# Kernel optimization log

Hardware: AMD Instinct MI355X
Metric: run time of the kernel (lower is better)

The kernel has to match this reference:

```python
import jax, jax.numpy as jnp
import numpy as np

B, S, D, H, CLIP = 4, 1024, 1024, 16, 64
DH = D // H

def setup_inputs() -> dict:
    key = jax.random.key(0)
    ks = jax.random.split(key, 10)
    sc = 1.0 / np.sqrt(D)
    return {
        "queries": jax.random.normal(ks[0], (B, S, D), jnp.float32),
        "keys": jax.random.normal(ks[1], (B, S, D), jnp.float32),
        "values": jax.random.normal(ks[2], (B, S, D), jnp.float32),
        "valid_lens": jax.random.randint(ks[3], (B,), 0, S),
        "Wq": jax.random.normal(ks[4], (D, D), jnp.float32) * sc,
        "Wk": jax.random.normal(ks[5], (D, D), jnp.float32) * sc,
        "Wv": jax.random.normal(ks[6], (D, D), jnp.float32) * sc,
        "Wo": jax.random.normal(ks[7], (D, D), jnp.float32) * sc,
        "rpr_k": jax.random.normal(ks[8], (2 * CLIP + 1, DH), jnp.float32),
        "rpr_v": jax.random.normal(ks[9], (2 * CLIP + 1, DH), jnp.float32),
    }

def reference(queries, keys, values, valid_lens, Wq, Wk, Wv, Wo, rpr_k, rpr_v):
    # project and split heads: [B,S,D] -> [B,H,S,DH]
    def split(x, W):
        return (x @ W).reshape(B, S, H, DH).transpose(0, 2, 1, 3)
    q = split(queries, Wq)
    k = split(keys, Wk)
    v = split(values, Wv)
    # relative position indices [S,S] in [0, 2*CLIP]
    dist = jnp.arange(S)[None, :] - jnp.arange(S)[:, None]
    dist = jnp.clip(dist, -CLIP, CLIP) + CLIP
    pos_k = rpr_k[dist]  # [S,S,DH]
    pos_v = rpr_v[dist]  # [S,S,DH]
    # content scores + relative-position key bias
    scores = jnp.einsum('bhqd,bhkd->bhqk', q, k)
    scores = scores + jnp.einsum('bhqd,qkd->bhqk', q, pos_k)
    scores = scores / jnp.sqrt(jnp.asarray(DH, q.dtype))
    # masked softmax: positions >= valid_len set to -1e6 (matches torch code)
    key_mask = jnp.arange(S)[None, None, None, :] < valid_lens[:, None, None, None]
    scores = jnp.where(key_mask, scores, jnp.asarray(-1e6, scores.dtype))
    attn = jax.nn.softmax(scores, axis=-1)  # [B,H,S,S]
    # value aggregation + relative-position value bias
    out = jnp.einsum('bhqk,bhkd->bhqd', attn, v)
    out = out + jnp.einsum('bhqk,qkd->bhqd', attn, pos_v)
    out = out.transpose(0, 2, 1, 3).reshape(B, S, D)
    return out @ Wo
```

## Files before the change

kernel.cpp:

```cpp
#include <hip/hip_runtime.h>
#include <stdint.h>
#include <math.h>

#define BB 4
#define SS 1024
#define DD 1024
#define HH 16
#define DHH 64
#define NCLIP 64
#define NCC 129
#define NCP 160
#define QRSTR 148
#define M0F 20.0f

typedef __bf16 bf16;
typedef __bf16 bf16x8 __attribute__((ext_vector_type(8)));
typedef float f32x4 __attribute__((ext_vector_type(4)));

__device__ __forceinline__ void gload_lds16(const void* g, void* l) {
  __builtin_amdgcn_global_load_lds((const __attribute__((address_space(1))) void*)g,
                                   (__attribute__((address_space(3))) void*)l, 16, 0, 0);
}

struct TpArgs { const float* w[4]; bf16* wt[4]; };
__global__ __launch_bounds__(256) void transpose_pack_w(TpArgs args) {
  const float* __restrict__ W = args.w[blockIdx.z];
  bf16* __restrict__ Wt = args.wt[blockIdx.z];
  __shared__ float tile[32][33];
  int tx = threadIdx.x, ty = threadIdx.y;
  int n0 = blockIdx.x * 32, k0 = blockIdx.y * 32;
#pragma unroll
  for (int i = 0; i < 4; i++)
    tile[ty + i * 8][tx] = W[(size_t)(k0 + ty + i * 8) * DD + n0 + tx];
  __syncthreads();
#pragma unroll
  for (int i = 0; i < 4; i++)
    Wt[(size_t)(n0 + ty + i * 8) * DD + k0 + tx] = (bf16)tile[tx][ty + i * 8];
}

struct CvtArgs { const float* in[3]; bf16* out[3]; int skip[3]; };
__global__ __launch_bounds__(256) void f32_to_bf16_3(CvtArgs args, const int* __restrict__ vlens) {
  const int z = blockIdx.z;
  if (args.skip[z]) {
    int row0 = (blockIdx.x * 2) & 1023;
    int b = (blockIdx.x * 2) >> 10;
    int vl = vlens[b];
    if (vl > 0 && row0 >= vl) return;
  }
  const float* __restrict__ in = args.in[z];
  bf16* __restrict__ out = args.out[z];
  size_t i = ((size_t)blockIdx.x * 256 + threadIdx.x) * 8;
  f32x4 v0 = *(const f32x4*)(in + i);
  f32x4 v1 = *(const f32x4*)(in + i + 4);
  bf16x8 o;
#pragma unroll
  for (int j = 0; j < 4; j++) { o[j] = (bf16)v0[j]; o[j + 4] = (bf16)v1[j]; }
  *(bf16x8*)(out + i) = o;
}

struct GemmArgs { const bf16* a[3]; const bf16* bt[3]; void* c[3]; float sc[3]; int skip[3]; };
template <bool SPLIT>
__global__ __launch_bounds__(256) void gemm128(GemmArgs args, const int* __restrict__ vlens) {
  const int z = blockIdx.z;
  const int m0 = blockIdx.y * 128, n0 = blockIdx.x * 128;
  if (args.skip[z]) {
    int vl = vlens[m0 >> 10];
    if (vl > 0 && (m0 & 1023) >= vl) return;
  }
  const bf16* __restrict__ A  = args.a[z];
  const bf16* __restrict__ Bt = args.bt[z];
  void* __restrict__ Cv = args.c[z];
  const float scale = args.sc[z];
  __shared__ __align__(16) bf16 As[128][32];
  __shared__ __align__(16) bf16 Bs[128][32];
  const int tid = threadIdx.x, lane = tid & 63, wv = tid >> 6;
  const int wr = wv >> 1, wc = wv & 1;
  const int l15 = lane & 15, l4 = lane >> 4;
  const int srow = lane >> 2, scol = (lane & 3) * 8;
  f32x4 z4 = {0.f, 0.f, 0.f, 0.f};
  f32x4 acc[4][4];
#pragma unroll
  for (int i = 0; i < 4; i++)
#pragma unroll
    for (int j = 0; j < 4; j++) acc[i][j] = z4;

  for (int k0 = 0; k0 < DD; k0 += 32) {
    gload_lds16(A  + (size_t)(m0 + wv * 16 + srow) * DD + k0 + scol,      &As[wv * 16][0]);
    gload_lds16(A  + (size_t)(m0 + 64 + wv * 16 + srow) * DD + k0 + scol, &As[64 + wv * 16][0]);
    gload_lds16(Bt + (size_t)(n0 + wv * 16 + srow) * DD + k0 + scol,      &Bs[wv * 16][0]);
    gload_lds16(Bt + (size_t)(n0 + 64 + wv * 16 + srow) * DD + k0 + scol, &Bs[64 + wv * 16][0]);
    __syncthreads();
    bf16x8 af[4], bfv[4];
#pragma unroll
    for (int i = 0; i < 4; i++) {
      af[i]  = *(const bf16x8*)&As[wr * 64 + i * 16 + l15][l4 * 8];
      bfv[i] = *(const bf16x8*)&Bs[wc * 64 + i * 16 + l15][l4 * 8];
    }
#pragma unroll
    for (int mi = 0; mi < 4; mi++)
#pragma unroll
      for (int ni = 0; ni < 4; ni++)
        acc[mi][ni] = __builtin_amdgcn_mfma_f32_16x16x32_bf16(af[mi], bfv[ni], acc[mi][ni], 0, 0, 0);
    __syncthreads();
  }
#pragma unroll
  for (int mi = 0; mi < 4; mi++)
#pragma unroll
    for (int ni = 0; ni < 4; ni++)
#pragma unroll
      for (int r = 0; r < 4; r++) {
        int m = m0 + wr * 64 + mi * 16 + l4 * 4 + r;
        int n = n0 + wc * 64 + ni * 16 + l15;
        float val = acc[mi][ni][r] * scale;
        if (SPLIT) {
          ((bf16*)Cv)[((((size_t)(m >> 10) * HH + (n >> 6)) * SS) + (m & 1023)) * DHH + (n & 63)] =
              (bf16)val;
        } else {
          ((float*)Cv)[(size_t)m * DD + n] = val;
        }
      }
}

__global__ __launch_bounds__(256) void gemm_bf16_final(const bf16* __restrict__ A,
                                                       const bf16* __restrict__ Bt,
                                                       float* __restrict__ C) {
  __shared__ __align__(16) bf16 As[64][32];
  __shared__ __align__(16) bf16 Bs[128][32];
  const int tid = threadIdx.x, lane = tid & 63, wv = tid >> 6;
  const int l15 = lane & 15, l4 = lane >> 4;
  const int m0 = blockIdx.y * 64, n0 = blockIdx.x * 128;
  const int srow = lane >> 2, scol = (lane & 3) * 8;
  f32x4 z4 = {0.f, 0.f, 0.f, 0.f};
  f32x4 acc[4][2];
#pragma unroll
  for (int i = 0; i < 4; i++) { acc[i][0] = z4; acc[i][1] = z4; }

  for (int k0 = 0; k0 < DD; k0 += 32) {
    gload_lds16(A + (size_t)(m0 + wv * 16 + srow) * DD + k0 + scol, &As[wv * 16][0]);
    gload_lds16(Bt + (size_t)(n0 + wv * 32 + srow) * DD + k0 + scol, &Bs[wv * 32][0]);
    gload_lds16(Bt + (size_t)(n0 + wv * 32 + 16 + srow) * DD + k0 + scol, &Bs[wv * 32 + 16][0]);
    __syncthreads();
    bf16x8 af[4], bfv[2];
#pragma unroll
    for (int i = 0; i < 4; i++) af[i] = *(const bf16x8*)&As[i * 16 + l15][l4 * 8];
#pragma unroll
    for (int i = 0; i < 2; i++) bfv[i] = *(const bf16x8*)&Bs[wv * 32 + i * 16 + l15][l4 * 8];
#pragma unroll
    for (int mi = 0; mi < 4; mi++)
#pragma unroll
      for (int ni = 0; ni < 2; ni++)
        acc[mi][ni] = __builtin_amdgcn_mfma_f32_16x16x32_bf16(af[mi], bfv[ni], acc[mi][ni], 0, 0, 0);
    __syncthreads();
  }
#pragma unroll
  for (int mi = 0; mi < 4; mi++)
#pragma unroll
    for (int ni = 0; ni < 2; ni++)
#pragma unroll
      for (int r = 0; r < 4; r++) {
        int m = m0 + mi * 16 + l4 * 4 + r;
        int n = n0 + wv * 32 + ni * 16 + l15;
        C[(size_t)m * DD + n] = acc[mi][ni][r];
      }
}

__global__ __launch_bounds__(256) void vh_transpose(const bf16* __restrict__ Vh,
                                                    bf16* __restrict__ VhT,
                                                    const int* __restrict__ vlens) {
  __shared__ bf16 til[64][65];
  int bh = blockIdx.y;
  int s0 = blockIdx.x * 64;
  int vl = vlens[bh >> 4];
  if (vl > 0 && s0 >= vl + 32) return;
  const bf16* src = Vh + (size_t)bh * SS * DHH + (size_t)s0 * DHH;
  for (int i = threadIdx.x; i < 64 * 64; i += 256) {
    int r = i >> 6, cc = i & 63;
    til[r][cc] = src[(size_t)r * DHH + cc];
  }
  __syncthreads();
  bf16* dst = VhT + (size_t)bh * DHH * SS + s0;
  for (int i = threadIdx.x; i < 64 * 64; i += 256) {
    int d = i >> 6, cc = i & 63;
    dst[(size_t)d * SS + cc] = til[cc][d];
  }
}

__global__ void prep_tables(const float* __restrict__ rpr_v, const float* __restrict__ rpr_k,
                            bf16* __restrict__ rvT, bf16* __restrict__ rkP) {
  int i = blockIdx.x * 256 + threadIdx.x;
  if (i < DHH * NCP) {
    int d = i / NCP, c = i - d * NCP;
    rvT[i] = (c < NCC) ? (bf16)rpr_v[(size_t)c * DHH + d] : (bf16)0.f;
  }
  if (i < 144 * 64) {
    rkP[i] = (i < NCC * DHH) ? (bf16)rpr_k[i] : (bf16)0.f;
  }
}

__global__ __launch_bounds__(256, 4) void attn_mfma(
    const bf16* __restrict__ Qh, const bf16* __restrict__ Kh, const bf16* __restrict__ VhT,
    const bf16* __restrict__ rkP, const int* __restrict__ valid_lens,
    const bf16* __restrict__ rvT, bf16* __restrict__ Obh) {
  __shared__ __align__(16) char arena[4][10240];
  const int tid = threadIdx.x, lane = tid & 63, w = tid >> 6;
  const int l15 = lane & 15, l4 = lane >> 4;
  const int b = blockIdx.z, h = blockIdx.y, bh = b * HH + h;
  const int q0 = blockIdx.x * 64 + w * 16;
  const int vlen = valid_lens[b];
  const float mval = (vlen == 0) ? 0.f : -30000.f;
  char* base = arena[w];
  bf16* QRs = (bf16*)base;
  _Float16* SBand = (_Float16*)(base + 4736);
  bf16* Pl = (bf16*)(base + 8832);

  const bf16* Qbase = Qh + ((size_t)bh * SS + q0) * DHH;
  bf16x8 qa0 = *(const bf16x8*)(Qbase + (size_t)l15 * DHH + l4 * 8);
  bf16x8 qa1 = *(const bf16x8*)(Qbase + (size_t)l15 * DHH + 32 + l4 * 8);
  const bf16* Kbase = Kh + (size_t)bh * SS * DHH;
  const bf16* Vbase = VhT + (size_t)bh * DHH * SS;
  f32x4 z = {0.f, 0.f, 0.f, 0.f};

#pragma unroll
  for (int ni = 0; ni < 9; ni++) {
    const bf16* rp = rkP + (size_t)(ni * 16 + l15) * DHH + l4 * 8;
    bf16x8 b0 = *(const bf16x8*)(rp);
    bf16x8 b1 = *(const bf16x8*)(rp + 32);
    f32x4 acc = __builtin_amdgcn_mfma_f32_16x16x32_bf16(qa0, b0, z, 0, 0, 0);
    acc = __builtin_amdgcn_mfma_f32_16x16x32_bf16(qa1, b1, acc, 0, 0, 0);
#pragma unroll
    for (int r = 0; r < 4; r++)
      QRs[(l4 * 4 + r) * QRSTR + ni * 16 + l15] = (bf16)acc[r];
  }
  {
    _Float16 ninf = (_Float16)(-65504.f);
    for (int i = lane; i < 16 * 128; i += 64) SBand[i] = ninf;
  }

  float biasLo[4], biasHi[4];
#pragma unroll
  for (int r = 0; r < 4; r++) {
    biasLo[r] = (float)QRs[(l4 * 4 + r) * QRSTR + 0];
    biasHi[r] = (float)QRs[(l4 * 4 + r) * QRSTR + 128];
  }

  float l_lane[4], slo[4], shi[4];
#pragma unroll
  for (int r = 0; r < 4; r++) { l_lane[r] = 0.f; slo[r] = 0.f; shi[r] = 0.f; }
  f32x4 acco[4];
#pragma unroll
  for (int i = 0; i < 4; i++) acco[i] = z;

  const int kf = (vlen > 0) ? (vlen & ~31) : 0;
  const int kte = (vlen > 0) ? ((vlen + 31) & ~31) : SS;
  int bs = q0 - 94; bs = (bs < 0) ? 0 : ((bs + 31) & ~31);
  int be = (q0 + 110) & ~31; if (be > SS) be = SS;
  const int p1 = (bs < kf) ? bs : kf;
  const int p2 = (be < kf) ? be : kf;

#define QK_LOADS                                                              \
    const bf16* kp = Kbase + (size_t)(ks + l15) * DHH + l4 * 8;               \
    bf16x8 kf00 = *(const bf16x8*)(kp);                                       \
    bf16x8 kf01 = *(const bf16x8*)(kp + 32);                                  \
    bf16x8 kf10 = *(const bf16x8*)(kp + 16 * DHH);                            \
    bf16x8 kf11 = *(const bf16x8*)(kp + 16 * DHH + 32);                       \
    f32x4 a0 = __builtin_amdgcn_mfma_f32_16x16x32_bf16(qa0, kf00, z, 0, 0, 0);\
    a0 = __builtin_amdgcn_mfma_f32_16x16x32_bf16(qa1, kf01, a0, 0, 0, 0);     \
    f32x4 a1 = __builtin_amdgcn_mfma_f32_16x16x32_bf16(qa0, kf10, z, 0, 0, 0);\
    a1 = __builtin_amdgcn_mfma_f32_16x16x32_bf16(qa1, kf11, a1, 0, 0, 0);

#define PV_STEP                                                               \
    bf16x8 pa = *(const bf16x8*)&Pl[l15 * 40 + l4 * 8];                       \
    const bf16* vp = Vbase + (size_t)l15 * SS + ks + l4 * 8;                  \
    acco[0] = __builtin_amdgcn_mfma_f32_16x16x32_bf16(pa, *(const bf16x8*)(vp), acco[0], 0, 0, 0);                    \
    acco[1] = __builtin_amdgcn_mfma_f32_16x16x32_bf16(pa, *(const bf16x8*)(vp + (size_t)16 * SS), acco[1], 0, 0, 0);  \
    acco[2] = __builtin_amdgcn_mfma_f32_16x16x32_bf16(pa, *(const bf16x8*)(vp + (size_t)32 * SS), acco[2], 0, 0, 0);  \
    acco[3] = __builtin_amdgcn_mfma_f32_16x16x32_bf16(pa, *(const bf16x8*)(vp + (size_t)48 * SS), acco[3], 0, 0, 0);

  for (int ks = 0; ks < p1; ks += 32) {
    QK_LOADS
#pragma unroll
    for (int sub = 0; sub < 2; sub++) {
      const f32x4 a = sub ? a1 : a0;
#pragma unroll
      for (int r = 0; r < 4; r++) {
        float p = __expf(a[r] + biasLo[r] - M0F);
        l_lane[r] += p; slo[r] += p;
        Pl[(l4 * 4 + r) * 40 + sub * 16 + l15] = (bf16)p;
      }
    }
    PV_STEP
  }
  for (int ks = p1; ks < p2; ks += 32) {
    QK_LOADS
#pragma unroll
    for (int sub = 0; sub < 2; sub++) {
      const f32x4 a = sub ? a1 : a0;
      const int kg = ks + sub * 16 + l15;
#pragma unroll
      for (int r = 0; r < 4; r++) {
        const int qloc = l4 * 4 + r;
        int dlt = kg - q0 - qloc;
        int c = (dlt < -NCLIP ? -NCLIP : (dlt > NCLIP ? NCLIP : dlt)) + NCLIP;
        float s = a[r] + (float)QRs[qloc * QRSTR + c];
        if (dlt > -64 && dlt < 64) SBand[qloc * 128 + dlt + 63] = (_Float16)s;
        float p = __expf(s - M0F);
        l_lane[r] += p;
        slo[r] += (dlt <= -64) ? p : 0.f;
        shi[r] += (dlt >= 64) ? p : 0.f;
        Pl[qloc * 40 + sub * 16 + l15] = (bf16)p;
      }
    }
    PV_STEP
  }
  for (int ks = p2; ks < kf; ks += 32) {
    QK_LOADS
#pragma unroll
    for (int sub = 0; sub < 2; sub++) {
      const f32x4 a = sub ? a1 : a0;
#pragma unroll
      for (int r = 0; r < 4; r++) {
        float p = __expf(a[r] + biasHi[r] - M0F);
        l_lane[r] += p; shi[r] += p;
        Pl[(l4 * 4 + r) * 40 + sub * 16 + l15] = (bf16)p;
      }
    }
    PV_STEP
  }
  for (int ks = kf; ks < kte; ks += 32) {
    const int rel = ks - q0;
    const int mode = (rel <= -95) ? 0 : (rel >= 79) ? 1 : 2;
    QK_LOADS
#pragma unroll
    for (int sub = 0; sub < 2; sub++) {
      const f32x4 a = sub ? a1 : a0;
      const int kg = ks + sub * 16 + l15;
      const bool msk = (kg >= vlen);
      if (mode == 0) {
#pragma unroll
        for (int r = 0; r < 4; r++) {
          float s = msk ? mval : (a[r] + biasLo[r]);
          float p = __expf(s - M0F);
          l_lane[r] += p; slo[r] += p;
          Pl[(l4 * 4 + r) * 40 + sub * 16 + l15] = (bf16)p;
        }
      } else if (mode == 1) {
#pragma unroll
        for (int r = 0; r < 4; r++) {
          float s = msk ? mval : (a[r] + biasHi[r]);
          float p = __expf(s - M0F);
          l_lane[r] += p; shi[r] += p;
          Pl[(l4 * 4 + r) * 40 + sub * 16 + l15] = (bf16)p;
        }
      } else {
#pragma unroll
        for (int r = 0; r < 4; r++) {
          const int qloc = l4 * 4 + r;
          int dlt = kg - q0 - qloc;
          int c = (dlt < -NCLIP ? -NCLIP : (dlt > NCLIP ? NCLIP : dlt)) + NCLIP;
          float s = a[r] + (float)QRs[qloc * QRSTR + c];
          if (msk) s = mval;
          if (dlt > -64 && dlt < 64) SBand[qloc * 128 + dlt + 63] = (_Float16)s;
          float p = __expf(s - M0F);
          l_lane[r] += p;
          slo[r] += (dlt <= -64) ? p : 0.f;
          shi[r] += (dlt >= 64) ? p : 0.f;
          Pl[qloc * 40 + sub * 16 + l15] = (bf16)p;
        }
      }
    }
    PV_STEP
  }
#undef QK_LOADS
#undef PV_STEP

  float* li_s   = (float*)(base + 8832);
  float* a0_s   = (float*)(base + 8896);
  float* a128_s = (float*)(base + 8960);
  float li_r[4];
#pragma unroll
  for (int r = 0; r < 4; r++) {
    const int qloc = l4 * 4 + r;
    float lt = l_lane[r], so = slo[r], sh = shi[r];
    lt += __shfl_xor(lt, 1, 64); so += __shfl_xor(so, 1, 64); sh += __shfl_xor(sh, 1, 64);
    lt += __shfl_xor(lt, 2, 64); so += __shfl_xor(so, 2, 64); sh += __shfl_xor(sh, 2, 64);
    lt += __shfl_xor(lt, 4, 64); so += __shfl_xor(so, 4, 64); sh += __shfl_xor(sh, 4, 64);
    lt += __shfl_xor(lt, 8, 64); so += __shfl_xor(so, 8, 64); sh += __shfl_xor(sh, 8, 64);
    float li = 1.f / lt;
    li_r[r] = li;
    if (l15 == 0) { li_s[qloc] = li; a0_s[qloc] = so * li; a128_s[qloc] = sh * li; }
  }
  bf16* AWs = (bf16*)base;
  for (int row = 0; row < 16; row++) {
    float li = li_s[row], a0 = a0_s[row], a128 = a128_s[row];
#pragma unroll
    for (int j = 0; j < 3; j++) {
      int c = lane + 64 * j;
      if (c < 160) {
        float val;
        if (c == 0) val = a0;
        else if (c == 128) val = a128;
        else if (c < 128) val = __expf((float)SBand[row * 128 + c - 1] - M0F) * li;
        else val = 0.f;
        AWs[row * 168 + c] = (bf16)val;
      }
    }
  }
  f32x4 acc2[4];
#pragma unroll
  for (int i = 0; i < 4; i++) acc2[i] = z;
#pragma unroll
  for (int kk = 0; kk < 5; kk++) {
    bf16x8 af = *(const bf16x8*)&AWs[l15 * 168 + kk * 32 + l4 * 8];
#pragma unroll
    for (int ni = 0; ni < 4; ni++) {
      bf16x8 bv = *(const bf16x8*)(rvT + (size_t)(ni * 16 + l15) * NCP + kk * 32 + l4 * 8);
      acc2[ni] = __builtin_amdgcn_mfma_f32_16x16x32_bf16(af, bv, acc2[ni], 0, 0, 0);
    }
  }
#pragma unroll
  for (int ni = 0; ni < 4; ni++)
#pragma unroll
    for (int r = 0; r < 4; r++) {
      int qg = q0 + l4 * 4 + r;
      Obh[((size_t)b * SS + qg) * DD + h * DHH + ni * 16 + l15] =
          (bf16)(acco[ni][r] * li_r[r] + acc2[ni][r]);
    }
}

extern "C" void kernel_launch(void* const* d_in, const int* in_sizes, int n_in,
                              void* d_out, int out_size, void* d_ws, size_t ws_size,
                              hipStream_t stream) {
  (void)in_sizes; (void)n_in; (void)out_size; (void)ws_size;
  const float* queries = (const float*)d_in[0];
  const float* keys    = (const float*)d_in[1];
  const float* values  = (const float*)d_in[2];
  const int*   vlens   = (const int*)d_in[3];
  const float* Wq = (const float*)d_in[4];
  const float* Wk = (const float*)d_in[5];
  const float* Wv = (const float*)d_in[6];
  const float* Wo = (const float*)d_in[7];
  const float* rpr_k = (const float*)d_in[8];
  const float* rpr_v = (const float*)d_in[9];

  char* ws = (char*)d_ws;
  const size_t MB = 1024 * 1024;
  bf16* Wtq  = (bf16*)(ws + 0 * MB);
  bf16* Wtk  = (bf16*)(ws + 2 * MB);
  bf16* Wtv  = (bf16*)(ws + 4 * MB);
  bf16* Wto  = (bf16*)(ws + 6 * MB);
  bf16* Qh   = (bf16*)(ws + 8 * MB);
  bf16* Kh   = (bf16*)(ws + 16 * MB);
  bf16* Vh   = (bf16*)(ws + 24 * MB);
  bf16* VhT  = (bf16*)(ws + 32 * MB);
  bf16* Qb   = (bf16*)(ws + 40 * MB);
  bf16* Kb   = (bf16*)(ws + 48 * MB);
  bf16* Vb   = (bf16*)(ws + 56 * MB);
  bf16* Obh  = (bf16*)(ws + 64 * MB);
  bf16* rvT  = (bf16*)(ws + 72 * MB);
  bf16* rkP  = (bf16*)(ws + 73 * MB);

  TpArgs tp; tp.w[0] = Wq; tp.w[1] = Wk; tp.w[2] = Wv; tp.w[3] = Wo;
  tp.wt[0] = Wtq; tp.wt[1] = Wtk; tp.wt[2] = Wtv; tp.wt[3] = Wto;
  transpose_pack_w<<<dim3(32, 32, 4), dim3(32, 8), 0, stream>>>(tp);

  CvtArgs cv; cv.in[0] = queries; cv.in[1] = keys; cv.in[2] = values;
  cv.out[0] = Qb; cv.out[1] = Kb; cv.out[2] = Vb;
  cv.skip[0] = 0; cv.skip[1] = 1; cv.skip[2] = 1;
  f32_to_bf16_3<<<dim3(2048, 1, 3), 256, 0, stream>>>(cv, vlens);

  GemmArgs gp;
  gp.a[0] = Qb; gp.a[1] = Kb; gp.a[2] = Vb;
  gp.bt[0] = Wtq; gp.bt[1] = Wtk; gp.bt[2] = Wtv;
  gp.c[0] = (void*)Qh; gp.c[1] = (void*)Kh; gp.c[2] = (void*)Vh;
  gp.sc[0] = 0.125f; gp.sc[1] = 1.0f; gp.sc[2] = 1.0f;
  gp.skip[0] = 0; gp.skip[1] = 1; gp.skip[2] = 1;
  gemm128<true><<<dim3(8, 32, 3), 256, 0, stream>>>(gp, vlens);

  vh_transpose<<<dim3(16, 64), 256, 0, stream>>>(Vh, VhT, vlens);
  prep_tables<<<dim3(40), 256, 0, stream>>>(rpr_v, rpr_k, rvT, rkP);
  attn_mfma<<<dim3(16, HH, BB), 256, 0, stream>>>(Qh, Kh, VhT, rkP, vlens, rvT, Obh);
  gemm_bf16_final<<<dim3(8, 64), 256, 0, stream>>>(Obh, Wto, (float*)d_out);
}
```

Before: 127.7 us.

## Split attention key range across wave pairs and merge partials via LDS atomics

```diff
diff --git a/kernel.cpp b/kernel.cpp
--- a/kernel.cpp
+++ b/kernel.cpp
@@ -201,17 +201,22 @@
     const bf16* __restrict__ Qh, const bf16* __restrict__ Kh, const bf16* __restrict__ VhT,
     const bf16* __restrict__ rkP, const int* __restrict__ valid_lens,
     const bf16* __restrict__ rvT, bf16* __restrict__ Obh) {
-  __shared__ __align__(16) char arena[4][10240];
+  __shared__ __align__(16) char arena[2][15744];
   const int tid = threadIdx.x, lane = tid & 63, w = tid >> 6;
+  const int pair = w >> 1, khalf = w & 1;
   const int l15 = lane & 15, l4 = lane >> 4;
   const int b = blockIdx.z, h = blockIdx.y, bh = b * HH + h;
-  const int q0 = blockIdx.x * 64 + w * 16;
+  const int q0 = blockIdx.x * 32 + pair * 16;
   const int vlen = valid_lens[b];
   const float mval = (vlen == 0) ? 0.f : -30000.f;
-  char* base = arena[w];
+  char* base = arena[pair];
   bf16* QRs = (bf16*)base;
-  _Float16* SBand = (_Float16*)(base + 4736);
-  bf16* Pl = (bf16*)(base + 8832);
+  bf16* Pl = (bf16*)(base + 4736 + khalf * 1280);
+  _Float16* SBand = (_Float16*)(base + 7296);
+  float* Oacc = (float*)(base + 11392);
+  float* lsum_l  = (float*)(base + 15488);
+  float* lsum_lo = (float*)(base + 15552);
+  float* lsum_hi = (float*)(base + 15616);
 
   const bf16* Qbase = Qh + ((size_t)bh * SS + q0) * DHH;
   bf16x8 qa0 = *(const bf16x8*)(Qbase + (size_t)l15 * DHH + l4 * 8);
@@ -220,8 +225,7 @@
   const bf16* Vbase = VhT + (size_t)bh * DHH * SS;
   f32x4 z = {0.f, 0.f, 0.f, 0.f};
 
-#pragma unroll
-  for (int ni = 0; ni < 9; ni++) {
+  for (int ni = khalf ? 5 : 0; ni < (khalf ? 9 : 5); ni++) {
     const bf16* rp = rkP + (size_t)(ni * 16 + l15) * DHH + l4 * 8;
     bf16x8 b0 = *(const bf16x8*)(rp);
     bf16x8 b1 = *(const bf16x8*)(rp + 32);
@@ -233,8 +237,11 @@
   }
   {
     _Float16 ninf = (_Float16)(-65504.f);
-    for (int i = lane; i < 16 * 128; i += 64) SBand[i] = ninf;
-  }
+    for (int i = lane + khalf * 1024; i < khalf * 1024 + 1024; i += 64) SBand[i] = ninf;
+    for (int i = lane + khalf * 64; i < 1024; i += 128) Oacc[i] = 0.f;
+    if (khalf == 0 && lane < 48) lsum_l[lane] = 0.f;
+  }
+  __syncthreads();
 
   float biasLo[4], biasHi[4];
 #pragma unroll
@@ -250,12 +257,17 @@
 #pragma unroll
   for (int i = 0; i < 4; i++) acco[i] = z;
 
-  const int kf = (vlen > 0) ? (vlen & ~31) : 0;
   const int kte = (vlen > 0) ? ((vlen + 31) & ~31) : SS;
+  const int kf  = (vlen > 0) ? (vlen & ~31) : 0;
   int bs = q0 - 94; bs = (bs < 0) ? 0 : ((bs + 31) & ~31);
   int be = (q0 + 110) & ~31; if (be > SS) be = SS;
-  const int p1 = (bs < kf) ? bs : kf;
-  const int p2 = (be < kf) ? be : kf;
+  const int P1 = (bs < kf) ? bs : kf;
+  const int P2 = (be < kf) ? be : kf;
+  const int kmid = ((kte + 63) >> 6) << 5;
+  const int kb = khalf ? kmid : 0;
+  const int ke = khalf ? kte : kmid;
+#define IMAX(a, bq) ((a) > (bq) ? (a) : (bq))
+#define IMIN(a, bq) ((a) < (bq) ? (a) : (bq))
 
 #define QK_LOADS                                                              \
     const bf16* kp = Kbase + (size_t)(ks + l15) * DHH + l4 * 8;               \
@@ -276,7 +288,7 @@
     acco[2] = __builtin_amdgcn_mfma_f32_16x16x32_bf16(pa, *(const bf16x8*)(vp + (size_t)32 * SS), acco[2], 0, 0, 0);  \
     acco[3] = __builtin_amdgcn_mfma_f32_16x16x32_bf16(pa, *(const bf16x8*)(vp + (size_t)48 * SS), acco[3], 0, 0, 0);
 
-  for (int ks = 0; ks < p1; ks += 32) {
+  for (int ks = kb, e = IMIN(P1, ke); ks < e; ks += 32) {
     QK_LOADS
 #pragma unroll
     for (int sub = 0; sub < 2; sub++) {
@@ -290,7 +302,7 @@
     }
     PV_STEP
   }
-  for (int ks = p1; ks < p2; ks += 32) {
+  for (int ks = IMAX(kb, P1), e = IMIN(P2, ke); ks < e; ks += 32) {
     QK_LOADS
 #pragma unroll
     for (int sub = 0; sub < 2; sub++) {
@@ -312,7 +324,7 @@
     }
     PV_STEP
   }
-  for (int ks = p2; ks < kf; ks += 32) {
+  for (int ks = IMAX(kb, P2), e = IMIN(kf, ke); ks < e; ks += 32) {
     QK_LOADS
 #pragma unroll
     for (int sub = 0; sub < 2; sub++) {
@@ -326,7 +338,7 @@
     }
     PV_STEP
   }
-  for (int ks = kf; ks < kte; ks += 32) {
+  for (int ks = IMAX(kb, kf), e = IMIN(kte, ke); ks < e; ks += 32) {
     const int rel = ks - q0;
     const int mode = (rel <= -95) ? 0 : (rel >= 79) ? 1 : 2;
     QK_LOADS
@@ -373,10 +385,6 @@
 #undef QK_LOADS
 #undef PV_STEP
 
-  float* li_s   = (float*)(base + 8832);
-  float* a0_s   = (float*)(base + 8896);
-  float* a128_s = (float*)(base + 8960);
-  float li_r[4];
 #pragma unroll
   for (int r = 0; r < 4; r++) {
     const int qloc = l4 * 4 + r;
@@ -385,46 +393,62 @@
     lt += __shfl_xor(lt, 2, 64); so += __shfl_xor(so, 2, 64); sh += __shfl_xor(sh, 2, 64);
     lt += __shfl_xor(lt, 4, 64); so += __shfl_xor(so, 4, 64); sh += __shfl_xor(sh, 4, 64);
     lt += __shfl_xor(lt, 8, 64); so += __shfl_xor(so, 8, 64); sh += __shfl_xor(sh, 8, 64);
-    float li = 1.f / lt;
-    li_r[r] = li;
-    if (l15 == 0) { li_s[qloc] = li; a0_s[qloc] = so * li; a128_s[qloc] = sh * li; }
-  }
+    if (l15 == 0) {
+      atomicAdd(&lsum_l[qloc], lt);
+      atomicAdd(&lsum_lo[qloc], so);
+      atomicAdd(&lsum_hi[qloc], sh);
+    }
+#pragma unroll
+    for (int ni = 0; ni < 4; ni++)
+      atomicAdd(&Oacc[qloc * 64 + ni * 16 + l15], acco[ni][r]);
+  }
+  __syncthreads();
+
   bf16* AWs = (bf16*)base;
-  for (int row = 0; row < 16; row++) {
-    float li = li_s[row], a0 = a0_s[row], a128 = a128_s[row];
+  for (int row = khalf * 8; row < khalf * 8 + 8; row++) {
+    float li = 1.f / lsum_l[row];
+    float a0v = lsum_lo[row] * li, a128v = lsum_hi[row] * li;
 #pragma unroll
     for (int j = 0; j < 3; j++) {
       int c = lane + 64 * j;
       if (c < 160) {
         float val;
-        if (c == 0) val = a0;
-        else if (c == 128) val = a128;
+        if (c == 0) val = a0v;
+        else if (c == 128) val = a128v;
         else if (c < 128) val = __expf((float)SBand[row * 128 + c - 1] - M0F) * li;
         else val = 0.f;
         AWs[row * 168 + c] = (bf16)val;
       }
     }
   }
-  f32x4 acc2[4];
-#pragma unroll
-  for (int i = 0; i < 4; i++) acc2[i] = z;
-#pragma unroll
-  for (int kk = 0; kk < 5; kk++) {
-    bf16x8 af = *(const bf16x8*)&AWs[l15 * 168 + kk * 32 + l4 * 8];
-#pragma unroll
-    for (int ni = 0; ni < 4; ni++) {
-      bf16x8 bv = *(const bf16x8*)(rvT + (size_t)(ni * 16 + l15) * NCP + kk * 32 + l4 * 8);
-      acc2[ni] = __builtin_amdgcn_mfma_f32_16x16x32_bf16(af, bv, acc2[ni], 0, 0, 0);
-    }
-  }
-#pragma unroll
-  for (int ni = 0; ni < 4; ni++)
-#pragma unroll
-    for (int r = 0; r < 4; r++) {
-      int qg = q0 + l4 * 4 + r;
-      Obh[((size_t)b * SS + qg) * DD + h * DHH + ni * 16 + l15] =
-          (bf16)(acco[ni][r] * li_r[r] + acc2[ni][r]);
-    }
+  __syncthreads();
+
+  if (khalf == 0) {
+    f32x4 acc2[4];
+#pragma unroll
+    for (int i = 0; i < 4; i++) acc2[i] = z;
+#pragma unroll
+    for (int kk = 0; kk < 5; kk++) {
+      bf16x8 af = *(const bf16x8*)&AWs[l15 * 168 + kk * 32 + l4 * 8];
+#pragma unroll
+      for (int ni = 0; ni < 4; ni++) {
+        bf16x8 bv = *(const bf16x8*)(rvT + (size_t)(ni * 16 + l15) * NCP + kk * 32 + l4 * 8);
+        acc2[ni] = __builtin_amdgcn_mfma_f32_16x16x32_bf16(af, bv, acc2[ni], 0, 0, 0);
+      }
+    }
+    float li_r[4];
+#pragma unroll
+    for (int r = 0; r < 4; r++) li_r[r] = 1.f / lsum_l[l4 * 4 + r];
+#pragma unroll
+    for (int ni = 0; ni < 4; ni++)
+#pragma unroll
+      for (int r = 0; r < 4; r++) {
+        const int qloc = l4 * 4 + r;
+        int qg = q0 + qloc;
+        float val = Oacc[qloc * 64 + ni * 16 + l15] * li_r[r] + acc2[ni][r];
+        Obh[((size_t)b * SS + qg) * DD + h * DHH + ni * 16 + l15] = (bf16)val;
+      }
+  }
 }
 
 extern "C" void kernel_launch(void* const* d_in, const int* in_sizes, int n_in,
@@ -478,6 +502,6 @@
 
   vh_transpose<<<dim3(16, 64), 256, 0, stream>>>(Vh, VhT, vlens);
   prep_tables<<<dim3(40), 256, 0, stream>>>(rpr_v, rpr_k, rvT, rkP);
-  attn_mfma<<<dim3(16, HH, BB), 256, 0, stream>>>(Qh, Kh, VhT, rkP, vlens, rvT, Obh);
+  attn_mfma<<<dim3(32, HH, BB), 256, 0, stream>>>(Qh, Kh, VhT, rkP, vlens, rvT, Obh);
   gemm_bf16_final<<<dim3(8, 64), 256, 0, stream>>>(Obh, Wto, (float*)d_out);
 }
```

Result: slower. 161.9 us (+26.8%).

## Stage K/V tiles in shared LDS across waves via async global-to-LDS loads

Applied to the files above, without the earlier changes.

```diff
diff --git a/kernel.cpp b/kernel.cpp
--- a/kernel.cpp
+++ b/kernel.cpp
@@ -197,10 +197,12 @@
   }
 }
 
-__global__ __launch_bounds__(256, 4) void attn_mfma(
+__global__ __launch_bounds__(256, 3) void attn_mfma(
     const bf16* __restrict__ Qh, const bf16* __restrict__ Kh, const bf16* __restrict__ VhT,
     const bf16* __restrict__ rkP, const int* __restrict__ valid_lens,
     const bf16* __restrict__ rvT, bf16* __restrict__ Obh) {
+  __shared__ __align__(16) bf16 Ks[32][64];
+  __shared__ __align__(16) bf16 Vs[64][32];
   __shared__ __align__(16) char arena[4][10240];
   const int tid = threadIdx.x, lane = tid & 63, w = tid >> 6;
   const int l15 = lane & 15, l4 = lane >> 4;
@@ -250,115 +252,95 @@
 #pragma unroll
   for (int i = 0; i < 4; i++) acco[i] = z;
 
-  const int kf = (vlen > 0) ? (vlen & ~31) : 0;
+  const int ksw0 = (l4 ^ (l15 & 7)) * 8;
+  const int ksw1 = ((l4 + 4) ^ (l15 & 7)) * 8;
+  const int vsw  = (l4 ^ (l15 & 3)) * 8;
+  const int krow = w * 8 + (lane >> 3);
+  const int kch  = ((lane & 7) ^ (krow & 7)) * 8;
+  const int vd   = w * 16 + (lane >> 2);
+  const int vch  = ((lane & 3) ^ (vd & 3)) * 8;
+
+  const int kfb = (vlen > 0) ? (vlen & ~31) : 0;
   const int kte = (vlen > 0) ? ((vlen + 31) & ~31) : SS;
   int bs = q0 - 94; bs = (bs < 0) ? 0 : ((bs + 31) & ~31);
   int be = (q0 + 110) & ~31; if (be > SS) be = SS;
-  const int p1 = (bs < kf) ? bs : kf;
-  const int p2 = (be < kf) ? be : kf;
-
-#define QK_LOADS                                                              \
-    const bf16* kp = Kbase + (size_t)(ks + l15) * DHH + l4 * 8;               \
-    bf16x8 kf00 = *(const bf16x8*)(kp);                                       \
-    bf16x8 kf01 = *(const bf16x8*)(kp + 32);                                  \
-    bf16x8 kf10 = *(const bf16x8*)(kp + 16 * DHH);                            \
-    bf16x8 kf11 = *(const bf16x8*)(kp + 16 * DHH + 32);                       \
-    f32x4 a0 = __builtin_amdgcn_mfma_f32_16x16x32_bf16(qa0, kf00, z, 0, 0, 0);\
-    a0 = __builtin_amdgcn_mfma_f32_16x16x32_bf16(qa1, kf01, a0, 0, 0, 0);     \
-    f32x4 a1 = __builtin_amdgcn_mfma_f32_16x16x32_bf16(qa0, kf10, z, 0, 0, 0);\
+
+  for (int ks = 0; ks < kte; ks += 32) {
+    gload_lds16(Kbase + (size_t)(ks + krow) * DHH + kch, &Ks[w * 8][0]);
+    gload_lds16(Vbase + (size_t)vd * SS + ks + vch, &Vs[w * 16][0]);
+    __syncthreads();
+    bf16x8 kf00 = *(const bf16x8*)&Ks[l15][ksw0];
+    bf16x8 kf01 = *(const bf16x8*)&Ks[l15][ksw1];
+    bf16x8 kf10 = *(const bf16x8*)&Ks[16 + l15][ksw0];
+    bf16x8 kf11 = *(const bf16x8*)&Ks[16 + l15][ksw1];
+    f32x4 a0 = __builtin_amdgcn_mfma_f32_16x16x32_bf16(qa0, kf00, z, 0, 0, 0);
+    a0 = __builtin_amdgcn_mfma_f32_16x16x32_bf16(qa1, kf01, a0, 0, 0, 0);
+    f32x4 a1 = __builtin_amdgcn_mfma_f32_16x16x32_bf16(qa0, kf10, z, 0, 0, 0);
     a1 = __builtin_amdgcn_mfma_f32_16x16x32_bf16(qa1, kf11, a1, 0, 0, 0);
 
-#define PV_STEP                                                               \
-    bf16x8 pa = *(const bf16x8*)&Pl[l15 * 40 + l4 * 8];                       \
-    const bf16* vp = Vbase + (size_t)l15 * SS + ks + l4 * 8;                  \
-    acco[0] = __builtin_amdgcn_mfma_f32_16x16x32_bf16(pa, *(const bf16x8*)(vp), acco[0], 0, 0, 0);                    \
-    acco[1] = __builtin_amdgcn_mfma_f32_16x16x32_bf16(pa, *(const bf16x8*)(vp + (size_t)16 * SS), acco[1], 0, 0, 0);  \
-    acco[2] = __builtin_amdgcn_mfma_f32_16x16x32_bf16(pa, *(const bf16x8*)(vp + (size_t)32 * SS), acco[2], 0, 0, 0);  \
-    acco[3] = __builtin_amdgcn_mfma_f32_16x16x32_bf16(pa, *(const bf16x8*)(vp + (size_t)48 * SS), acco[3], 0, 0, 0);
-
-  for (int ks = 0; ks < p1; ks += 32) {
-    QK_LOADS
-#pragma unroll
-    for (int sub = 0; sub < 2; sub++) {
-      const f32x4 a = sub ? a1 : a0;
-#pragma unroll
-      for (int r = 0; r < 4; r++) {
-        float p = __expf(a[r] + biasLo[r] - M0F);
-        l_lane[r] += p; slo[r] += p;
-        Pl[(l4 * 4 + r) * 40 + sub * 16 + l15] = (bf16)p;
-      }
-    }
-    PV_STEP
-  }
-  for (int ks = p1; ks < p2; ks += 32) {
-    QK_LOADS
-#pragma unroll
-    for (int sub = 0; sub < 2; sub++) {
-      const f32x4 a = sub ? a1 : a0;
-      const int kg = ks + sub * 16 + l15;
-#pragma unroll
-      for (int r = 0; r < 4; r++) {
-        const int qloc = l4 * 4 + r;
-        int dlt = kg - q0 - qloc;
-        int c = (dlt < -NCLIP ? -NCLIP : (dlt > NCLIP ? NCLIP : dlt)) + NCLIP;
-        float s = a[r] + (float)QRs[qloc * QRSTR + c];
-        if (dlt > -64 && dlt < 64) SBand[qloc * 128 + dlt + 63] = (_Float16)s;
-        float p = __expf(s - M0F);
-        l_lane[r] += p;
-        slo[r] += (dlt <= -64) ? p : 0.f;
-        shi[r] += (dlt >= 64) ? p : 0.f;
-        Pl[qloc * 40 + sub * 16 + l15] = (bf16)p;
-      }
-    }
-    PV_STEP
-  }
-  for (int ks = p2; ks < kf; ks += 32) {
-    QK_LOADS
-#pragma unroll
-    for (int sub = 0; sub < 2; sub++) {
-      const f32x4 a = sub ? a1 : a0;
-#pragma unroll
-      for (int r = 0; r < 4; r++) {
-        float p = __expf(a[r] + biasHi[r] - M0F);
-        l_lane[r] += p; shi[r] += p;
-        Pl[(l4 * 4 + r) * 40 + sub * 16 + l15] = (bf16)p;
-      }
-    }
-    PV_STEP
-  }
-  for (int ks = kf; ks < kte; ks += 32) {
-    const int rel = ks - q0;
-    const int mode = (rel <= -95) ? 0 : (rel >= 79) ? 1 : 2;
-    QK_LOADS
-#pragma unroll
-    for (int sub = 0; sub < 2; sub++) {
-      const f32x4 a = sub ? a1 : a0;
-      const int kg = ks + sub * 16 + l15;
-      const bool msk = (kg >= vlen);
-      if (mode == 0) {
+    if (ks >= kfb) {
+      const int rel = ks - q0;
+      const int mode = (rel <= -95) ? 0 : (rel >= 79) ? 1 : 2;
+#pragma unroll
+      for (int sub = 0; sub < 2; sub++) {
+        const f32x4 a = sub ? a1 : a0;
+        const int kg = ks + sub * 16 + l15;
+        const bool msk = (kg >= vlen);
+        if (mode == 0) {
+#pragma unroll
+          for (int r = 0; r < 4; r++) {
+            float s = msk ? mval : (a[r] + biasLo[r]);
+            float p = __expf(s - M0F);
+            l_lane[r] += p; slo[r] += p;
+            Pl[(l4 * 4 + r) * 40 + sub * 16 + l15] = (bf16)p;
+          }
+        } else if (mode == 1) {
+#pragma unroll
+          for (int r = 0; r < 4; r++) {
+            float s = msk ? mval : (a[r] + biasHi[r]);
+            float p = __expf(s - M0F);
+            l_lane[r] += p; shi[r] += p;
+            Pl[(l4 * 4 + r) * 40 + sub * 16 + l15] = (bf16)p;
+          }
+        } else {
+#pragma unroll
+          for (int r = 0; r < 4; r++) {
+            const int qloc = l4 * 4 + r;
+            int dlt = kg - q0 - qloc;
+            int c = (dlt < -NCLIP ? -NCLIP : (dlt > NCLIP ? NCLIP : dlt)) + NCLIP;
+            float s = a[r] + (float)QRs[qloc * QRSTR + c];
+            if (msk) s = mval;
+            if (dlt > -64 && dlt < 64) SBand[qloc * 128 + dlt + 63] = (_Float16)s;
+            float p = __expf(s - M0F);
+            l_lane[r] += p;
+            slo[r] += (dlt <= -64) ? p : 0.f;
+            shi[r] += (dlt >= 64) ? p : 0.f;
+            Pl[qloc * 40 + sub * 16 + l15] = (bf16)p;
+          }
+        }
+      }
+    } else if (ks < bs) {
+#pragma unroll
+      for (int sub = 0; sub < 2; sub++) {
+        const f32x4 a = sub ? a1 : a0;
 #pragma unroll
         for (int r = 0; r < 4; r++) {
-          float s = msk ? mval : (a[r] + biasLo[r]);
-          float p = __expf(s - M0F);
+          float p = __expf(a[r] + biasLo[r] - M0F);
           l_lane[r] += p; slo[r] += p;
           Pl[(l4 * 4 + r) * 40 + sub * 16 + l15] = (bf16)p;
         }
-      } else if (mode == 1) {
-#pragma unroll
-        for (int r = 0; r < 4; r++) {
-          float s = msk ? mval : (a[r] + biasHi[r]);
-          float p = __expf(s - M0F);
-          l_lane[r] += p; shi[r] += p;
-          Pl[(l4 * 4 + r) * 40 + sub * 16 + l15] = (bf16)p;
-        }
-      } else {
+      }
+    } else if (ks < be) {
+#pragma unroll
+      for (int sub = 0; sub < 2; sub++) {
+        const f32x4 a = sub ? a1 : a0;
+        const int kg = ks + sub * 16 + l15;
 #pragma unroll
         for (int r = 0; r < 4; r++) {
           const int qloc = l4 * 4 + r;
           int dlt = kg - q0 - qloc;
           int c = (dlt < -NCLIP ? -NCLIP : (dlt > NCLIP ? NCLIP : dlt)) + NCLIP;
           float s = a[r] + (float)QRs[qloc * QRSTR + c];
-          if (msk) s = mval;
           if (dlt > -64 && dlt < 64) SBand[qloc * 128 + dlt + 63] = (_Float16)s;
           float p = __expf(s - M0F);
           l_lane[r] += p;
@@ -367,11 +349,26 @@
           Pl[qloc * 40 + sub * 16 + l15] = (bf16)p;
         }
       }
+    } else {
+#pragma unroll
+      for (int sub = 0; sub < 2; sub++) {
+        const f32x4 a = sub ? a1 : a0;
+#pragma unroll
+        for (int r = 0; r < 4; r++) {
+          float p = __expf(a[r] + biasHi[r] - M0F);
+          l_lane[r] += p; shi[r] += p;
+          Pl[(l4 * 4 + r) * 40 + sub * 16 + l15] = (bf16)p;
+        }
+      }
     }
-    PV_STEP
-  }
-#undef QK_LOADS
-#undef PV_STEP
+
+    bf16x8 pa = *(const bf16x8*)&Pl[l15 * 40 + l4 * 8];
+    acco[0] = __builtin_amdgcn_mfma_f32_16x16x32_bf16(pa, *(const bf16x8*)&Vs[l15][vsw], acco[0], 0, 0, 0);
+    acco[1] = __builtin_amdgcn_mfma_f32_16x16x32_bf16(pa, *(const bf16x8*)&Vs[16 + l15][vsw], acco[1], 0, 0, 0);
+    acco[2] = __builtin_amdgcn_mfma_f32_16x16x32_bf16(pa, *(const bf16x8*)&Vs[32 + l15][vsw], acco[2], 0, 0, 0);
+    acco[3] = __builtin_amdgcn_mfma_f32_16x16x32_bf16(pa, *(const bf16x8*)&Vs[48 + l15][vsw], acco[3], 0, 0, 0);
+    __syncthreads();
+  }
 
   float* li_s   = (float*)(base + 8832);
   float* a0_s   = (float*)(base + 8896);
```

Measured after the change: 114.5 us, median of 2. 10.3% less time.
